# Kernel optimization log

Hardware: AMD Instinct MI355X
Metric: run time of the kernel (lower is better)

## Reference

```python
import jax, jax.numpy as jnp
import numpy as np

B, N, C_IN, C_OUT = 16, 1024, 256, 256
POOL_RATIO = 0.5  # pooling_ration


def setup_inputs() -> dict:
    key = jax.random.key(0)
    k0, k1, k2, k3 = jax.random.split(key, 4)
    x = jax.random.normal(k0, (B, N, C_IN), dtype=jnp.float32)
    # sparse-ish dense adjacency (as the module stores adj densely)
    adj = (jax.random.uniform(k1, (B, N, N)) < 0.02).astype(jnp.float32)
    mask = jnp.ones((B, N), dtype=jnp.int32)
    n_nodes = jnp.full((B,), N, dtype=jnp.int32)
    stdv = 1.0 / np.sqrt(C_IN)
    W = jax.random.uniform(k2, (C_IN, C_OUT), minval=-stdv, maxval=stdv, dtype=jnp.float32)
    b = jnp.zeros((C_OUT,), dtype=jnp.float32)
    pooling = jax.random.uniform(k3, (C_OUT, 1), minval=-1.0, maxval=1.0, dtype=jnp.float32)
    return {"x": x, "adj": adj, "mask": mask, "n_nodes": n_nodes, "W": W, "b": b, "pooling": pooling}


def reference(x, adj, mask, n_nodes, W, b, pooling):
    # GraphConvolutionLayer: adj @ (x W) + b   (standard Kipf GCN layer)
    h = jnp.einsum('bnm,bmc->bnc', adj, x @ W) + b          # [B,N,C_OUT]
    Bm, Nm, C = h.shape
    # projection score y = (h @ pooling) / ||pooling||
    y = (h.reshape(Bm * Nm, C) @ pooling).reshape(Bm, Nm)
    y = y / jnp.sqrt(jnp.sum(pooling ** 2))
    # ascending sort indices
    idx = jnp.argsort(y, axis=1)                            # [B,N]
    n_remove = (n_nodes.astype(jnp.float32) * (1.0 - POOL_RATIO)).astype(jnp.int32)
    new_n_nodes = n_nodes - n_remove
    # vectorized equivalent of the per-batch loop: among currently-masked nodes
    # (in ascending-score order), zero out the first n_remove[b] of them.
    m_sorted = jnp.take_along_axis(mask, idx, axis=1)       # mask gathered in sorted order
    rank = jnp.cumsum(m_sorted, axis=1) - m_sorted          # exclusive rank among masked
    remove = (m_sorted == 1) & (rank < n_remove[:, None])
    new_sorted = jnp.where(remove, 0, m_sorted)
    inv = jnp.argsort(idx, axis=1)                          # inverse permutation
    new_mask = jnp.take_along_axis(new_sorted, inv, axis=1)  # [B,N] int
    mf = new_mask.astype(h.dtype)
    x_out = h * jnp.tanh(y)[:, :, None] * mf[:, :, None]
    adj_out = mf[:, :, None] * adj * mf[:, None, :]
    return x_out, adj_out, new_mask, new_n_nodes
```

## Files before the change

### kernel.cpp

```cpp
#include <hip/hip_runtime.h>
#include <math.h>

#define Bsz 16
#define Nn  1024

#define ADJ_OFF    (16*1024*256)
#define MASK_OFF   (ADJ_OFF + 16*1024*1024)
#define NN_OFF     (MASK_OFF + 16*1024)

typedef unsigned long long u64;
typedef unsigned short u16;
typedef short bf16x8 __attribute__((ext_vector_type(8)));
typedef float f32x4  __attribute__((ext_vector_type(4)));

static __device__ inline u16 f2bf(float f) {
    unsigned u = __float_as_uint(f);
    u += 0x7fffu + ((u >> 16) & 1u);
    return (u16)(u >> 16);
}

__global__ __launch_bounds__(256) void k1(const float* __restrict__ x,
                                          const float* __restrict__ W,
                                          const float* __restrict__ pool,
                                          u16* __restrict__ XB,
                                          u16* __restrict__ WT,
                                          float* __restrict__ Z) {
    int bid = blockIdx.x, t = threadIdx.x, lane = t & 63, wid = t >> 6;
    if (bid < 256) {
        __shared__ float sp[256];
        __shared__ float swp[256];
        sp[t] = pool[t];
        __syncthreads();
        float acc = 0.f;
        const float* wr = W + t * 256;
        for (int j = 0; j < 256; j += 4) {
            float4 w4 = *(const float4*)&wr[j];
            acc = fmaf(w4.x, sp[j], fmaf(w4.y, sp[j + 1],
                  fmaf(w4.z, sp[j + 2], fmaf(w4.w, sp[j + 3], acc))));
        }
        swp[t] = acc;
        __syncthreads();
        const float* w4p = &swp[lane * 4];
        float wx = w4p[0], wy = w4p[1], wz = w4p[2], ww = w4p[3];
        int base = bid * 64 + wid * 16;
        #pragma unroll 1
        for (int rb = 0; rb < 4; ++rb) {
            float4 v[4];
            #pragma unroll
            for (int k = 0; k < 4; ++k)
                v[k] = ((const float4*)(x + (size_t)(base + rb * 4 + k) * 256))[lane];
            #pragma unroll
            for (int k = 0; k < 4; ++k) {
                int row = base + rb * 4 + k;
                ushort4 o;
                o.x = f2bf(v[k].x); o.y = f2bf(v[k].y); o.z = f2bf(v[k].z); o.w = f2bf(v[k].w);
                ((ushort4*)(XB + (size_t)row * 256))[lane] = o;
                float a = fmaf(v[k].x, wx, fmaf(v[k].y, wy, fmaf(v[k].z, wz, v[k].w * ww)));
                for (int off = 32; off > 0; off >>= 1) a += __shfl_down(a, off, 64);
                if (lane == 0) Z[row] = a;
            }
        }
    } else {
        __shared__ float sT[64][65];
        int bt = bid - 256;
        int tr = (bt >> 2) * 64, tc = (bt & 3) * 64;
        #pragma unroll
        for (int p = 0; p < 4; ++p) {
            int r = p * 16 + (t >> 4), c = (t & 15) * 4;
            float4 w = *(const float4*)&W[(size_t)(tr + r) * 256 + tc + c];
            sT[r][c] = w.x; sT[r][c + 1] = w.y; sT[r][c + 2] = w.z; sT[r][c + 3] = w.w;
        }
        __syncthreads();
        #pragma unroll
        for (int p = 0; p < 2; ++p) {
            int nl = p * 32 + (t >> 3), kl = (t & 7) * 8;
            u16 tmp[8];
            #pragma unroll
            for (int j = 0; j < 8; ++j) tmp[j] = f2bf(sT[kl + j][nl]);
            *(int4*)&WT[(size_t)(tc + nl) * 256 + tr + kl] = *(const int4*)tmp;
        }
    }
}

__global__ __launch_bounds__(256) void k2(const u16* __restrict__ XB,
                                          const u16* __restrict__ WT,
                                          const float* __restrict__ adj,
                                          const float* __restrict__ Z,
                                          u16* __restrict__ XWBT,
                                          u16* __restrict__ AB,
                                          float* __restrict__ Y) {
    int t = threadIdx.x, lane = t & 63, wid = t >> 6;
    if (blockIdx.x < 256) {
        __shared__ short sA[128][72];
        __shared__ short sB[128][72];
        int bm = blockIdx.x >> 1, bn = blockIdx.x & 1;
        int wr = (wid >> 1) * 64, wc = (wid & 1) * 64;
        int fm = lane & 15, fq = lane >> 4;

        f32x4 acc[4][4];
        #pragma unroll
        for (int i = 0; i < 4; ++i)
            #pragma unroll
            for (int j = 0; j < 4; ++j)
                acc[i][j] = (f32x4){0.f, 0.f, 0.f, 0.f};

        int sr = t >> 1, half = (t & 1) * 32;
        const u16* gA = XB + ((size_t)(bm * 128 + sr)) * 256 + half;
        const u16* gB = WT + ((size_t)(bn * 128 + sr)) * 256 + half;

        for (int kt = 0; kt < 4; ++kt) {
            __syncthreads();
            #pragma unroll
            for (int q = 0; q < 4; ++q) {
                *(int4*)&sA[sr][half + q * 8] = *(const int4*)&gA[kt * 64 + q * 8];
                *(int4*)&sB[sr][half + q * 8] = *(const int4*)&gB[kt * 64 + q * 8];
            }
            __syncthreads();
            #pragma unroll
            for (int ks = 0; ks < 64; ks += 32) {
                bf16x8 af[4], bfv[4];
                #pragma unroll
                for (int i = 0; i < 4; ++i)
                    af[i] = *(const bf16x8*)&sA[wr + i * 16 + fm][ks + fq * 8];
                #pragma unroll
                for (int j = 0; j < 4; ++j)
                    bfv[j] = *(const bf16x8*)&sB[wc + j * 16 + fm][ks + fq * 8];
                #pragma unroll
                for (int i = 0; i < 4; ++i)
                    #pragma unroll
                    for (int j = 0; j < 4; ++j)
                        acc[i][j] = __builtin_amdgcn_mfma_f32_16x16x32_bf16(af[i], bfv[j], acc[i][j], 0, 0, 0);
            }
        }
        int b = bm >> 3;
        #pragma unroll
        for (int i = 0; i < 4; ++i) {
            int rloc = (bm & 7) * 128 + wr + i * 16 + fq * 4;
            #pragma unroll
            for (int j = 0; j < 4; ++j) {
                int c = bn * 128 + wc + j * 16 + fm;
                u16 tmp[4];
                #pragma unroll
                for (int r = 0; r < 4; ++r) tmp[r] = f2bf(acc[i][j][r]);
                *(unsigned long long*)&XWBT[(size_t)b * 262144 + (size_t)c * 1024 + rloc] =
                    *(const unsigned long long*)tmp;
            }
        }
    } else {
        int g = blockIdx.x - 256;
        int b = g >> 6, grp = g & 63;
        __shared__ float sZ[1024];
        ((float4*)sZ)[t] = ((const float4*)(Z + (b << 10)))[t];
        __syncthreads();
        const float* z0 = &sZ[lane * 4];
        #pragma unroll 1
        for (int rr = 0; rr < 4; ++rr) {
            int row = (b << 10) + grp * 16 + wid * 4 + rr;
            const float4* ar = (const float4*)(adj + (size_t)row * 1024);
            float4 v0 = ar[lane], v1 = ar[64 + lane], v2 = ar[128 + lane], v3 = ar[192 + lane];
            u16* abr = AB + (size_t)row * 1024;
            ushort4 o0, o1, o2, o3;
            o0.x = f2bf(v0.x); o0.y = f2bf(v0.y); o0.z = f2bf(v0.z); o0.w = f2bf(v0.w);
            o1.x = f2bf(v1.x); o1.y = f2bf(v1.y); o1.z = f2bf(v1.z); o1.w = f2bf(v1.w);
            o2.x = f2bf(v2.x); o2.y = f2bf(v2.y); o2.z = f2bf(v2.z); o2.w = f2bf(v2.w);
            o3.x = f2bf(v3.x); o3.y = f2bf(v3.y); o3.z = f2bf(v3.z); o3.w = f2bf(v3.w);
            ((ushort4*)abr)[lane] = o0;
            ((ushort4*)abr)[64 + lane] = o1;
            ((ushort4*)abr)[128 + lane] = o2;
            ((ushort4*)abr)[192 + lane] = o3;
            float a = v0.x * z0[0] + v0.y * z0[1] + v0.z * z0[2] + v0.w * z0[3];
            a += v1.x * z0[256] + v1.y * z0[257] + v1.z * z0[258] + v1.w * z0[259];
            a += v2.x * z0[512] + v2.y * z0[513] + v2.z * z0[514] + v2.w * z0[515];
            a += v3.x * z0[768] + v3.y * z0[769] + v3.z * z0[770] + v3.w * z0[771];
            for (int off = 32; off > 0; off >>= 1) a += __shfl_down(a, off, 64);
            if (lane == 0) Y[row] = a;
        }
    }
}

__device__ inline u64 shfl_xor_u64(u64 v, int m) {
    int lo = __shfl_xor((int)(v & 0xffffffffULL), m, 64);
    int hi = __shfl_xor((int)(v >> 32), m, 64);
    return ((u64)(unsigned)hi << 32) | (unsigned)lo;
}

__global__ __launch_bounds__(1024) void k3(const float* __restrict__ Y,
                                           const int* __restrict__ maskIn,
                                           const int* __restrict__ nNodes,
                                           const float* __restrict__ bias,
                                           const float* __restrict__ pool,
                                           float* __restrict__ SCALE,
                                           float* __restrict__ NM,
                                           float* __restrict__ newN,
                                           u64* __restrict__ NMBITS) {
    __shared__ u64 s[1024];
    __shared__ int wsum[16];
    __shared__ int nmLoc[1024];
    __shared__ float redb[4], redq[4];
    __shared__ float sBP, sINV;

    int b = blockIdx.x, t = threadIdx.x, lane = t & 63, wid = t >> 6;
    int base = b << 10;

    if (t < 256) {
        float pv = pool[t];
        float bv = bias[t] * pv;
        float qv = pv * pv;
        for (int off = 32; off > 0; off >>= 1) {
            bv += __shfl_down(bv, off, 64);
            qv += __shfl_down(qv, off, 64);
        }
        if (lane == 0) { redb[wid] = bv; redq[wid] = qv; }
    }
    __syncthreads();
    if (t == 0) {
        sBP  = redb[0] + redb[1] + redb[2] + redb[3];
        sINV = 1.0f / sqrtf(redq[0] + redq[1] + redq[2] + redq[3]);
    }

    float ky = Y[base + t];
    unsigned u = __float_as_uint(ky);
    u = (u & 0x80000000u) ? ~u : (u | 0x80000000u);
    u64 val = ((u64)u << 32) | (unsigned)t;

    for (int k = 2; k <= 1024; k <<= 1) {
        bool up = ((t & k) == 0);
        int j = k >> 1;
        for (; j >= 64; j >>= 1) {
            s[t] = val; __syncthreads();
            u64 p = s[t ^ j]; __syncthreads();
            bool keepMin = (up == ((t & j) == 0));
            bool pLess = p < val;
            val = (keepMin == pLess) ? p : val;
        }
        for (; j >= 1; j >>= 1) {
            u64 p = shfl_xor_u64(val, j);
            bool keepMin = (up == ((t & j) == 0));
            bool pLess = p < val;
            val = (keepMin == pLess) ? p : val;
        }
    }

    int idx = (int)(val & 1023u);
    int mval = maskIn[base + idx];
    int sc = mval;
    for (int off = 1; off < 64; off <<= 1) {
        int nv = __shfl_up(sc, off, 64);
        if (lane >= off) sc += nv;
    }
    if (lane == 63) wsum[wid] = sc;
    __syncthreads();
    int offset = 0;
    for (int w = 0; w < wid; ++w) offset += wsum[w];
    int rank = sc + offset - mval;
    int nn = nNodes[b];
    int nrem = (int)((float)nn * 0.5f);
    int nm = (mval == 1 && rank < nrem) ? 0 : mval;
    nmLoc[idx] = nm;
    NM[base + idx] = (float)nm;
    if (t == 0) newN[b] = (float)(nn - nrem);
    __syncthreads();

    int myNm = nmLoc[t];
    u64 bmask = __ballot(myNm != 0);
    if (lane == 0) NMBITS[b * 16 + wid] = bmask;
    float yr = Y[base + t];
    SCALE[base + t] = myNm ? tanhf((yr + sBP) * sINV) : 0.0f;
}

__global__ __launch_bounds__(256) void k4(const u16* __restrict__ AB,
                                          const u16* __restrict__ XWBT,
                                          const float* __restrict__ SCALE,
                                          const float* __restrict__ bias,
                                          const u64* __restrict__ NMBITS,
                                          float* __restrict__ XO,
                                          float* __restrict__ AO) {
    int t = threadIdx.x, lane = t & 63, wid = t >> 6;
    if (blockIdx.x < 256) {
        __shared__ short sA[128][72];
        __shared__ short sB[128][72];
        int idx = blockIdx.x;
        int bn = idx & 1, bmt = (idx >> 1) & 7, b = idx >> 4;
        int wr = (wid >> 1) * 64, wc = (wid & 1) * 64;
        int fm = lane & 15, fq = lane >> 4;

        f32x4 acc[4][4];
        #pragma unroll
        for (int i = 0; i < 4; ++i)
            #pragma unroll
            for (int j = 0; j < 4; ++j)
                acc[i][j] = (f32x4){0.f, 0.f, 0.f, 0.f};

        int sr = t >> 1, half = (t & 1) * 32;
        const u16* gA = AB + ((size_t)(b * 1024 + bmt * 128 + sr)) * 1024 + half;
        const u16* gB = XWBT + (size_t)b * 262144 + (size_t)(bn * 128 + sr) * 1024 + half;

        for (int kt = 0; kt < 16; ++kt) {
            __syncthreads();
            #pragma unroll
            for (int q = 0; q < 4; ++q) {
                *(int4*)&sA[sr][half + q * 8] = *(const int4*)&gA[kt * 64 + q * 8];
                *(int4*)&sB[sr][half + q * 8] = *(const int4*)&gB[kt * 64 + q * 8];
            }
            __syncthreads();
            #pragma unroll
            for (int ks = 0; ks < 64; ks += 32) {
                bf16x8 af[4], bfv[4];
                #pragma unroll
                for (int i = 0; i < 4; ++i)
                    af[i] = *(const bf16x8*)&sA[wr + i * 16 + fm][ks + fq * 8];
                #pragma unroll
                for (int j = 0; j < 4; ++j)
                    bfv[j] = *(const bf16x8*)&sB[wc + j * 16 + fm][ks + fq * 8];
                #pragma unroll
                for (int i = 0; i < 4; ++i)
                    #pragma unroll
                    for (int j = 0; j < 4; ++j)
                        acc[i][j] = __builtin_amdgcn_mfma_f32_16x16x32_bf16(af[i], bfv[j], acc[i][j], 0, 0, 0);
            }
        }
        float bj[4];
        #pragma unroll
        for (int j = 0; j < 4; ++j) bj[j] = bias[bn * 128 + wc + j * 16 + fm];
        int mb = (b << 10) + bmt * 128 + wr;
        #pragma unroll
        for (int i = 0; i < 4; ++i) {
            int m0 = mb + i * 16 + fq * 4;
            float s0 = SCALE[m0], s1 = SCALE[m0 + 1], s2 = SCALE[m0 + 2], s3 = SCALE[m0 + 3];
            #pragma unroll
            for (int j = 0; j < 4; ++j) {
                int c = bn * 128 + wc + j * 16 + fm;
                float* xo = XO + (size_t)m0 * 256 + c;
                xo[0]   = (acc[i][j][0] + bj[j]) * s0;
                xo[256] = (acc[i][j][1] + bj[j]) * s1;
                xo[512] = (acc[i][j][2] + bj[j]) * s2;
                xo[768] = (acc[i][j][3] + bj[j]) * s3;
            }
        }
    } else {
        int g = blockIdx.x - 256;
        int b = g >> 6, grp = g & 63;
        __shared__ u64 sBits[16];
        if (t < 16) sBits[t] = NMBITS[b * 16 + t];
        __syncthreads();
        int c0 = t * 4;
        u64 wb = sBits[c0 >> 6] >> (c0 & 63);
        float m0 = (wb & 1) ? 1.f : 0.f;
        float m1 = ((wb >> 1) & 1) ? 1.f : 0.f;
        float m2 = ((wb >> 2) & 1) ? 1.f : 0.f;
        float m3 = ((wb >> 3) & 1) ? 1.f : 0.f;
        #pragma unroll 1
        for (int r = 0; r < 16; ++r) {
            int rloc = grp * 16 + r;
            int nmRow = (int)((sBits[rloc >> 6] >> (rloc & 63)) & 1ULL);
            float4* aor = (float4*)(AO + (size_t)((b << 10) + rloc) * 1024);
            if (nmRow) {
                ushort4 ab = ((const ushort4*)(AB + (size_t)((b << 10) + rloc) * 1024))[t];
                float4 o;
                o.x = ab.x ? m0 : 0.f;
                o.y = ab.y ? m1 : 0.f;
                o.z = ab.z ? m2 : 0.f;
                o.w = ab.w ? m3 : 0.f;
                aor[t] = o;
            } else {
                aor[t] = make_float4(0.f, 0.f, 0.f, 0.f);
            }
        }
    }
}

extern "C" void kernel_launch(void* const* d_in, const int* in_sizes, int n_in,
                              void* d_out, int out_size, void* d_ws, size_t ws_size,
                              hipStream_t stream) {
    const float* x      = (const float*)d_in[0];
    const float* adj    = (const float*)d_in[1];
    const int*   mask   = (const int*)d_in[2];
    const int*   nnodes = (const int*)d_in[3];
    const float* W      = (const float*)d_in[4];
    const float* bias   = (const float*)d_in[5];
    const float* pool   = (const float*)d_in[6];

    float* out = (float*)d_out;
    float* XO  = out;
    float* AO  = out + ADJ_OFF;
    float* NM  = out + MASK_OFF;
    float* NNo = out + NN_OFF;

    char* w = (char*)d_ws;
    u16*   XB     = (u16*)(w);
    u16*   WT     = (u16*)(w + 8388608);
    u16*   XWBT   = (u16*)(w + 8519680);
    u16*   AB     = (u16*)(w + 16908288);
    float* Z      = (float*)(w + 50462720);
    float* Y      = (float*)(w + 50528256);
    float* SCALE  = (float*)(w + 50593792);
    u64*   NMBITS = (u64*)(w + 50659328);

    k1<<<272, 256, 0, stream>>>(x, W, pool, XB, WT, Z);
    k2<<<1280, 256, 0, stream>>>(XB, WT, adj, Z, XWBT, AB, Y);
    k3<<<Bsz, 1024, 0, stream>>>(Y, mask, nnodes, bias, pool, SCALE, NM, NNo, NMBITS);
    k4<<<1280, 256, 0, stream>>>(AB, XWBT, SCALE, bias, NMBITS, XO, AO);
}
```

Baseline: 208.0 us.

## Remap block-to-batch assignment for XCD locality, stage transposed store via LDS, add MFMA priority

Block indices in k2 and k4 are remapped so that consecutive blocks land on different batches modulo 8. The apparent aim is to keep each batch's tiles on a single XCD, so its L2 cache can reuse the shared operands. The transposed XWBT epilogue in k2 now stages the bf16 results through LDS and writes coalesced 16-byte rows instead of scattered 8-byte stores. s_setprio is also placed around the MFMA bursts so waves favour issuing matrix instructions. These add an extra LDS round trip and barriers in the epilogue.

New measurement: 207.6 us. No clear change (-0.2%).

```diff
diff --git a/kernel.cpp b/kernel.cpp
--- a/kernel.cpp
+++ b/kernel.cpp
@@ -91,9 +91,14 @@
                                           float* __restrict__ Y) {
     int t = threadIdx.x, lane = t & 63, wid = t >> 6;
     if (blockIdx.x < 256) {
-        __shared__ short sA[128][72];
-        __shared__ short sB[128][72];
-        int bm = blockIdx.x >> 1, bn = blockIdx.x & 1;
+        __shared__ __align__(16) short smem[2 * 128 * 72];
+        short (*sA)[72] = (short (*)[72])smem;
+        short (*sB)[72] = (short (*)[72])(smem + 128 * 72);
+        int idx = blockIdx.x;
+        int b  = (idx & 7) + ((idx >> 7) << 3);
+        int tl = (idx >> 3) & 15;
+        int bm = (b << 3) + (tl >> 1);
+        int bn = tl & 1;
         int wr = (wid >> 1) * 64, wc = (wid & 1) * 64;
         int fm = lane & 15, fq = lane >> 4;
 
@@ -125,30 +130,40 @@
                 #pragma unroll
                 for (int j = 0; j < 4; ++j)
                     bfv[j] = *(const bf16x8*)&sB[wc + j * 16 + fm][ks + fq * 8];
+                __builtin_amdgcn_s_setprio(1);
                 #pragma unroll
                 for (int i = 0; i < 4; ++i)
                     #pragma unroll
                     for (int j = 0; j < 4; ++j)
                         acc[i][j] = __builtin_amdgcn_mfma_f32_16x16x32_bf16(af[i], bfv[j], acc[i][j], 0, 0, 0);
-            }
-        }
-        int b = bm >> 3;
+                __builtin_amdgcn_s_setprio(0);
+            }
+        }
+        __syncthreads();
+        short (*sT)[136] = (short (*)[136])smem;
         #pragma unroll
         for (int i = 0; i < 4; ++i) {
-            int rloc = (bm & 7) * 128 + wr + i * 16 + fq * 4;
+            int m = wr + i * 16 + fq * 4;
             #pragma unroll
             for (int j = 0; j < 4; ++j) {
-                int c = bn * 128 + wc + j * 16 + fm;
-                u16 tmp[4];
-                #pragma unroll
-                for (int r = 0; r < 4; ++r) tmp[r] = f2bf(acc[i][j][r]);
-                *(unsigned long long*)&XWBT[(size_t)b * 262144 + (size_t)c * 1024 + rloc] =
-                    *(const unsigned long long*)tmp;
-            }
+                int c = wc + j * 16 + fm;
+                #pragma unroll
+                for (int r = 0; r < 4; ++r)
+                    sT[c][m + r] = (short)f2bf(acc[i][j][r]);
+            }
+        }
+        __syncthreads();
+        u16* dst = XWBT + (size_t)b * 262144 + (size_t)(bn * 128) * 1024 + (bm & 7) * 128;
+        int cl = t >> 4, mo = (t & 15) * 8;
+        #pragma unroll
+        for (int p = 0; p < 8; ++p) {
+            int c = p * 16 + cl;
+            *(int4*)&dst[(size_t)c * 1024 + mo] = *(const int4*)&sT[c][mo];
         }
     } else {
         int g = blockIdx.x - 256;
-        int b = g >> 6, grp = g & 63;
+        int b = (g & 7) + ((g >> 9) << 3);
+        int grp = (g >> 3) & 63;
         __shared__ float sZ[1024];
         ((float4*)sZ)[t] = ((const float4*)(Z + (b << 10)))[t];
         __syncthreads();
@@ -280,7 +295,9 @@
         __shared__ short sA[128][72];
         __shared__ short sB[128][72];
         int idx = blockIdx.x;
-        int bn = idx & 1, bmt = (idx >> 1) & 7, b = idx >> 4;
+        int b   = (idx & 7) + ((idx >> 7) << 3);
+        int tl  = (idx >> 3) & 15;
+        int bmt = tl >> 1, bn = tl & 1;
         int wr = (wid >> 1) * 64, wc = (wid & 1) * 64;
         int fm = lane & 15, fq = lane >> 4;
 
@@ -312,11 +329,13 @@
                 #pragma unroll
                 for (int j = 0; j < 4; ++j)
                     bfv[j] = *(const bf16x8*)&sB[wc + j * 16 + fm][ks + fq * 8];
+                __builtin_amdgcn_s_setprio(1);
                 #pragma unroll
                 for (int i = 0; i < 4; ++i)
                     #pragma unroll
                     for (int j = 0; j < 4; ++j)
                         acc[i][j] = __builtin_amdgcn_mfma_f32_16x16x32_bf16(af[i], bfv[j], acc[i][j], 0, 0, 0);
+                __builtin_amdgcn_s_setprio(0);
             }
         }
         float bj[4];
@@ -339,7 +358,8 @@
         }
     } else {
         int g = blockIdx.x - 256;
-        int b = g >> 6, grp = g & 63;
+        int b = (g & 7) + ((g >> 9) << 3);
+        int grp = (g >> 3) & 63;
         __shared__ u64 sBits[16];
         if (t < 16) sBits[t] = NMBITS[b * 16 + t];
         __syncthreads();
```
